# Kernel tuning notes

Measured on AMD Instinct MI355X. Metric: run time of the kernel, lower is better.

## Reference

```python
import jax, jax.numpy as jnp
import numpy as np

LN_EPS = 1e-5


def setup_inputs() -> dict:
    key = jax.random.key(0)
    ks = jax.random.split(key, 6)
    B, L, N, H, V = 4, 4, 2048, 64, 4
    x = jax.random.normal(ks[0], (B, N, H), dtype=jnp.float32)
    feature = jax.random.normal(ks[1], (B, N, 2), dtype=jnp.float32)
    adj = jax.random.uniform(ks[2], (B, L, N, N), dtype=jnp.float32)
    fc_w = jax.random.normal(ks[3], (H, H + 2), dtype=jnp.float32) * (1.0 / np.sqrt(H + 2))
    fc_b = jnp.zeros((H,), dtype=jnp.float32)
    ln_g = jnp.ones((H,), dtype=jnp.float32)
    ln_b = jnp.zeros((H,), dtype=jnp.float32)
    W = jax.random.normal(ks[4], (H, V, H), dtype=jnp.float32) * (1.0 / np.sqrt(H))
    a = jax.random.normal(ks[5], (L + 1, V), dtype=jnp.float32) * 0.5
    return {"x": x, "feature": feature, "adj": adj, "fc_w": fc_w, "fc_b": fc_b,
            "ln_g": ln_g, "ln_b": ln_b, "W": W, "a": a}


def reference(x, feature, adj, fc_w, fc_b, ln_g, ln_b, W, a):
    # x: [B,N,H], feature: [B,N,2], adj: [B,L,N,N]
    label_plus1 = a.shape[0]  # label_num + 1
    h = jnp.concatenate([x, feature], axis=2) @ fc_w.T + fc_b  # [B,N,H]
    mu = jnp.mean(h, axis=-1, keepdims=True)
    var = jnp.var(h, axis=-1, keepdims=True)
    h = (h - mu) / jnp.sqrt(var + LN_EPS) * ln_g + ln_b
    h = jnp.tanh(h)  # dropout inactive in eval mode
    # supports: identity relation (h itself) + one bmm per adjacency label
    prop = jnp.einsum('blnm,bmd->blnd', adj, h)            # [B,L,N,H]
    supports = jnp.concatenate([h[:, None], prop], axis=1)  # [B,L+1,N,H]
    # combine learned per-label weights: a @ W -> [L+1, H, H]
    M = jnp.einsum('lv,dve->lde', a, W)
    out = jnp.einsum('blnd,lde->bne', supports, M) / label_plus1  # sum over labels
    return out + x  # residual with original x
```

## Files before the change

kernel.cpp:

```cpp
#include <hip/hip_runtime.h>
#include <stdint.h>

#define BB 4
#define LL 4
#define NN 2048
#define HH 64

typedef __attribute__((ext_vector_type(4))) float  f32x4;
typedef __attribute__((ext_vector_type(8))) short  short8;

static __device__ __forceinline__ uint16_t f2bf(float f) {
    uint32_t u = __float_as_uint(f);
    u += 0x7FFFu + ((u >> 16) & 1u);
    return (uint16_t)(u >> 16);
}

__global__ __launch_bounds__(256) void prep_kernel(
    const float* __restrict__ x, const float* __restrict__ feat,
    const float* __restrict__ fc_w, const float* __restrict__ fc_b,
    const float* __restrict__ ln_g, const float* __restrict__ ln_b,
    const float* __restrict__ W, const float* __restrict__ a,
    float* __restrict__ out, uint16_t* __restrict__ zT)
{
    __shared__ float    sW[64 * 67];
    __shared__ uint16_t sM[5 * 64 * 64];

    const int tid = threadIdx.x;

    for (int i = tid; i < 64 * 66; i += 256) {
        int d = i / 66, k = i - d * 66;
        sW[d * 67 + k] = fc_w[i];
    }
    for (int i = tid; i < 5 * 64 * 64; i += 256) {
        int l = i >> 12;
        int d = (i >> 6) & 63;
        int e = i & 63;
        const float* wp = W + (size_t)(d * 4) * 64 + e;
        float acc = a[l * 4 + 0] * wp[0]   + a[l * 4 + 1] * wp[64]
                  + a[l * 4 + 2] * wp[128] + a[l * 4 + 3] * wp[192];
        sM[i] = f2bf(acc);
    }
    __syncthreads();

    const int wave = tid >> 6, lane = tid & 63;
    const int row0 = blockIdx.x * 32 + wave * 8;
    const int b    = row0 >> 11;
    const int m0   = row0 & 2047;

    const float fcb = fc_b[lane], lng = ln_g[lane], lnb = ln_b[lane];

    float xv[8], hv[8];
#pragma unroll
    for (int r = 0; r < 8; r++) {
        const int row = row0 + r;
        xv[r] = x[(size_t)row * 64 + lane];
        const float f0 = feat[row * 2 + 0];
        const float f1 = feat[row * 2 + 1];
        float acc = fcb;
#pragma unroll
        for (int k = 0; k < 64; k++)
            acc += __shfl(xv[r], k) * sW[lane * 67 + k];
        acc += f0 * sW[lane * 67 + 64] + f1 * sW[lane * 67 + 65];
        float s = acc, s2 = acc * acc;
#pragma unroll
        for (int off = 32; off > 0; off >>= 1) {
            s  += __shfl_xor(s,  off);
            s2 += __shfl_xor(s2, off);
        }
        const float mean = s * (1.0f / 64.0f);
        const float var  = s2 * (1.0f / 64.0f) - mean * mean;
        const float y = (acc - mean) * rsqrtf(var + 1e-5f) * lng + lnb;
        hv[r] = tanhf(y);
    }

    float accz[5][8];
#pragma unroll
    for (int l = 0; l < 5; l++)
#pragma unroll
        for (int r = 0; r < 8; r++) accz[l][r] = 0.0f;

    for (int d = 0; d < 64; d++) {
        float hb[8];
#pragma unroll
        for (int r = 0; r < 8; r++) hb[r] = __shfl(hv[r], d);
#pragma unroll
        for (int l = 0; l < 5; l++) {
            const float mv =
                __uint_as_float(((uint32_t)sM[(l << 12) + (d << 6) + lane]) << 16);
#pragma unroll
            for (int r = 0; r < 8; r++) accz[l][r] += hb[r] * mv;
        }
    }

#pragma unroll
    for (int r = 0; r < 8; r++)
        out[(size_t)(row0 + r) * 64 + lane] = xv[r] + 0.2f * accz[0][r];

#pragma unroll
    for (int l = 1; l < 5; l++) {
        uint32_t w0 = (uint32_t)f2bf(accz[l][0]) | ((uint32_t)f2bf(accz[l][1]) << 16);
        uint32_t w1 = (uint32_t)f2bf(accz[l][2]) | ((uint32_t)f2bf(accz[l][3]) << 16);
        uint32_t w2 = (uint32_t)f2bf(accz[l][4]) | ((uint32_t)f2bf(accz[l][5]) << 16);
        uint32_t w3 = (uint32_t)f2bf(accz[l][6]) | ((uint32_t)f2bf(accz[l][7]) << 16);
        uint4* dst = (uint4*)(zT + (((size_t)(b * 4 + (l - 1)) * 64 + lane) * 2048 + m0));
        *dst = make_uint4(w0, w1, w2, w3);
    }
}

__global__ __launch_bounds__(256) void gemm_kernel(
    const float* __restrict__ adj, const uint16_t* __restrict__ zT,
    float* __restrict__ out)
{
    __shared__ float sAcc[4][32 * 64];

    const int blk = blockIdx.x;
    const int rt  = blk & 63;
    const int b   = blk >> 6;

    const int wave = threadIdx.x >> 6;
    const int lane = threadIdx.x & 63;
    const int q    = lane >> 4;
    const int mr   = lane & 15;

    const int n0 = rt * 32;

    const float* adjBase = adj + ((size_t)(b * 4 + wave) * 2048) * 2048;
    const float* aRow0 = adjBase + (size_t)(n0 + mr) * 2048 + q * 8;
    const float* aRow1 = aRow0 + (size_t)16 * 2048;
    const uint16_t* zCol =
        zT + ((size_t)(b * 4 + wave) * 64 + mr) * 2048 + q * 8;

    f32x4 acc[2][4];
#pragma unroll
    for (int i = 0; i < 2; i++)
#pragma unroll
        for (int j = 0; j < 4; j++) acc[i][j] = (f32x4){0.f, 0.f, 0.f, 0.f};

    f32x4  af[2][2][2];
    short8 bq[2][4];

#define LOADSTEP(pp, s) do {                                                  \
        const float* _a0 = aRow0 + (s) * 32;                                  \
        const float* _a1 = aRow1 + (s) * 32;                                  \
        af[pp][0][0] = *(const f32x4*)(_a0);                                  \
        af[pp][0][1] = *(const f32x4*)(_a0 + 4);                              \
        af[pp][1][0] = *(const f32x4*)(_a1);                                  \
        af[pp][1][1] = *(const f32x4*)(_a1 + 4);                              \
        const uint16_t* _z = zCol + (s) * 32;                                 \
        bq[pp][0] = *(const short8*)(_z);                                     \
        bq[pp][1] = *(const short8*)(_z + 16 * 2048);                         \
        bq[pp][2] = *(const short8*)(_z + 32 * 2048);                         \
        bq[pp][3] = *(const short8*)(_z + 48 * 2048);                         \
    } while (0)

#define COMPUTE(pp) do {                                                      \
        short8 _fa0, _fa1;                                                    \
        _Pragma("unroll")                                                     \
        for (int j = 0; j < 4; j++) {                                         \
            _fa0[j]     = (short)f2bf(af[pp][0][0][j]);                       \
            _fa0[j + 4] = (short)f2bf(af[pp][0][1][j]);                       \
            _fa1[j]     = (short)f2bf(af[pp][1][0][j]);                       \
            _fa1[j + 4] = (short)f2bf(af[pp][1][1][j]);                       \
        }                                                                     \
        _Pragma("unroll")                                                     \
        for (int et = 0; et < 4; et++) {                                      \
            acc[0][et] = __builtin_amdgcn_mfma_f32_16x16x32_bf16(             \
                _fa0, bq[pp][et], acc[0][et], 0, 0, 0);                       \
            acc[1][et] = __builtin_amdgcn_mfma_f32_16x16x32_bf16(             \
                _fa1, bq[pp][et], acc[1][et], 0, 0, 0);                       \
        }                                                                     \
    } while (0)

    LOADSTEP(0, 0);
    for (int s = 0; s < 62; s += 2) {
        LOADSTEP(1, s + 1);
        COMPUTE(0);
        LOADSTEP(0, s + 2);
        COMPUTE(1);
    }
    LOADSTEP(1, 63);
    COMPUTE(0);
    COMPUTE(1);

#undef LOADSTEP
#undef COMPUTE

#pragma unroll
    for (int f = 0; f < 2; f++)
#pragma unroll
        for (int et = 0; et < 4; et++)
#pragma unroll
            for (int r = 0; r < 4; r++)
                sAcc[wave][(f * 16 + q * 4 + r) * 64 + et * 16 + mr] =
                    acc[f][et][r];
    __syncthreads();

    const int t    = threadIdx.x;
    const int row  = t >> 3;
    const int col0 = (t & 7) * 8;
    const int lo   = row * 64 + col0;
    float* op = out + ((size_t)b * 2048 + n0 + row) * 64 + col0;
#pragma unroll
    for (int p = 0; p < 2; p++) {
        f32x4 s = *(const f32x4*)&sAcc[0][lo + p * 4];
        s = s + *(const f32x4*)&sAcc[1][lo + p * 4];
        s = s + *(const f32x4*)&sAcc[2][lo + p * 4];
        s = s + *(const f32x4*)&sAcc[3][lo + p * 4];
        f32x4 o = *(f32x4*)(op + p * 4);
        o = o + 0.2f * s;
        *(f32x4*)(op + p * 4) = o;
    }
}

extern "C" void kernel_launch(void* const* d_in, const int* in_sizes, int n_in,
                              void* d_out, int out_size, void* d_ws, size_t ws_size,
                              hipStream_t stream) {
    const float* x    = (const float*)d_in[0];
    const float* feat = (const float*)d_in[1];
    const float* adj  = (const float*)d_in[2];
    const float* fc_w = (const float*)d_in[3];
    const float* fc_b = (const float*)d_in[4];
    const float* ln_g = (const float*)d_in[5];
    const float* ln_b = (const float*)d_in[6];
    const float* W    = (const float*)d_in[7];
    const float* a    = (const float*)d_in[8];

    float*    out = (float*)d_out;
    uint16_t* zT  = (uint16_t*)d_ws;

    prep_kernel<<<256, 256, 0, stream>>>(x, feat, fc_w, fc_b, ln_g, ln_b,
                                         W, a, out, zT);
    gemm_kernel<<<256, 256, 0, stream>>>(adj, zT, out);
}
```

Baseline: 444.2 us.

## Split GEMM K dimension across 8 waves, swizzle blocks, stage W in LDS

The adjacency GEMM now runs 512-thread blocks in which each label's K range is split across two waves. This doubles the waves in flight for the memory-bound stream over adj, and partial sums are reduced through a larger LDS buffer. Block indices are remapped so consecutive blocks spread across batches, which may change how work lands on the XCDs. The prep kernel first copies W into shared memory before building the combined label weights, at the cost of extra LDS and another barrier.

```diff
diff --git a/kernel.cpp b/kernel.cpp
--- a/kernel.cpp
+++ b/kernel.cpp
@@ -24,6 +24,7 @@
 {
     __shared__ float    sW[64 * 67];
     __shared__ uint16_t sM[5 * 64 * 64];
+    __shared__ float    sWt[64 * 4 * 64];
 
     const int tid = threadIdx.x;
 
@@ -31,11 +32,15 @@
         int d = i / 66, k = i - d * 66;
         sW[d * 67 + k] = fc_w[i];
     }
+    for (int i = tid; i < 64 * 4 * 64 / 4; i += 256)
+        ((f32x4*)sWt)[i] = ((const f32x4*)W)[i];
+    __syncthreads();
+
     for (int i = tid; i < 5 * 64 * 64; i += 256) {
         int l = i >> 12;
         int d = (i >> 6) & 63;
         int e = i & 63;
-        const float* wp = W + (size_t)(d * 4) * 64 + e;
+        const float* wp = sWt + d * 256 + e;
         float acc = a[l * 4 + 0] * wp[0]   + a[l * 4 + 1] * wp[64]
                   + a[l * 4 + 2] * wp[128] + a[l * 4 + 3] * wp[192];
         sM[i] = f2bf(acc);
@@ -107,28 +112,31 @@
     }
 }
 
-__global__ __launch_bounds__(256) void gemm_kernel(
+__global__ __launch_bounds__(512) void gemm_kernel(
     const float* __restrict__ adj, const uint16_t* __restrict__ zT,
     float* __restrict__ out)
 {
-    __shared__ float sAcc[4][32 * 64];
-
-    const int blk = blockIdx.x;
+    __shared__ float sAcc[8][32 * 64];
+
+    const int blk = (blockIdx.x & 7) * 32 + (blockIdx.x >> 3);
     const int rt  = blk & 63;
     const int b   = blk >> 6;
 
     const int wave = threadIdx.x >> 6;
+    const int l    = wave & 3;
+    const int kh   = wave >> 2;
     const int lane = threadIdx.x & 63;
     const int q    = lane >> 4;
     const int mr   = lane & 15;
 
     const int n0 = rt * 32;
-
-    const float* adjBase = adj + ((size_t)(b * 4 + wave) * 2048) * 2048;
-    const float* aRow0 = adjBase + (size_t)(n0 + mr) * 2048 + q * 8;
+    const int k0 = kh * 1024;
+
+    const float* adjBase = adj + ((size_t)(b * 4 + l) * 2048) * 2048;
+    const float* aRow0 = adjBase + (size_t)(n0 + mr) * 2048 + k0 + q * 8;
     const float* aRow1 = aRow0 + (size_t)16 * 2048;
     const uint16_t* zCol =
-        zT + ((size_t)(b * 4 + wave) * 64 + mr) * 2048 + q * 8;
+        zT + ((size_t)(b * 4 + l) * 64 + mr) * 2048 + k0 + q * 8;
 
     f32x4 acc[2][4];
 #pragma unroll
@@ -172,13 +180,13 @@
     } while (0)
 
     LOADSTEP(0, 0);
-    for (int s = 0; s < 62; s += 2) {
+    for (int s = 0; s < 30; s += 2) {
         LOADSTEP(1, s + 1);
         COMPUTE(0);
         LOADSTEP(0, s + 2);
         COMPUTE(1);
     }
-    LOADSTEP(1, 63);
+    LOADSTEP(1, 31);
     COMPUTE(0);
     COMPUTE(1);
 
@@ -196,20 +204,17 @@
     __syncthreads();
 
     const int t    = threadIdx.x;
-    const int row  = t >> 3;
-    const int col0 = (t & 7) * 8;
+    const int row  = t >> 4;
+    const int col0 = (t & 15) * 4;
     const int lo   = row * 64 + col0;
     float* op = out + ((size_t)b * 2048 + n0 + row) * 64 + col0;
-#pragma unroll
-    for (int p = 0; p < 2; p++) {
-        f32x4 s = *(const f32x4*)&sAcc[0][lo + p * 4];
-        s = s + *(const f32x4*)&sAcc[1][lo + p * 4];
-        s = s + *(const f32x4*)&sAcc[2][lo + p * 4];
-        s = s + *(const f32x4*)&sAcc[3][lo + p * 4];
-        f32x4 o = *(f32x4*)(op + p * 4);
-        o = o + 0.2f * s;
-        *(f32x4*)(op + p * 4) = o;
-    }
+    f32x4 s = *(const f32x4*)&sAcc[0][lo];
+#pragma unroll
+    for (int w = 1; w < 8; w++)
+        s = s + *(const f32x4*)&sAcc[w][lo];
+    f32x4 o = *(f32x4*)op;
+    o = o + 0.2f * s;
+    *(f32x4*)op = o;
 }
 
 extern "C" void kernel_launch(void* const* d_in, const int* in_sizes, int n_in,
@@ -230,5 +235,5 @@
 
     prep_kernel<<<256, 256, 0, stream>>>(x, feat, fc_w, fc_b, ln_g, ln_b,
                                          W, a, out, zT);
-    gemm_kernel<<<256, 256, 0, stream>>>(adj, zT, out);
-}
+    gemm_kernel<<<256, 512, 0, stream>>>(adj, zT, out);
+}
```

Result: no change. 441.2 us (-0.7%).
